# Kernel tuning notes

Hardware: AMD Instinct MI355X
Metric: run time of the kernel (lower is better)

Reference implementation:

```python
import jax, jax.numpy as jnp
import numpy as np

HEAD_NUM = 16
QKV_DIM = 32
EMB = 512
SQRT_EMB = 22.627416997969522  # sqrt(512)
LOGIT_CLIP = 10.0
BATCH, POMO, PROBLEM = 32, 256, 1024


def setup_inputs() -> dict:
    key = jax.random.key(0)
    ks = jax.random.split(key, 8)
    s = 0.02
    return {
        "encoded_nodes": jax.random.normal(ks[0], (BATCH, PROBLEM, EMB), jnp.float32),
        "encoded_q1": jax.random.normal(ks[1], (BATCH, POMO, EMB), jnp.float32),
        "encoded_last_node": jax.random.normal(ks[2], (BATCH, POMO, EMB), jnp.float32),
        "ninf_mask": jnp.zeros((BATCH, POMO, PROBLEM), jnp.float32),
        # weights stored [in, out] so y = x @ W (equiv. to torch Linear with W.T)
        "Wq_first": jax.random.normal(ks[3], (EMB, HEAD_NUM * QKV_DIM), jnp.float32) * s,
        "Wq_last": jax.random.normal(ks[4], (EMB, HEAD_NUM * QKV_DIM), jnp.float32) * s,
        "Wk": jax.random.normal(ks[5], (EMB, HEAD_NUM * QKV_DIM), jnp.float32) * s,
        "Wv": jax.random.normal(ks[6], (EMB, HEAD_NUM * QKV_DIM), jnp.float32) * s,
        "W_combine": jax.random.normal(ks[7], (HEAD_NUM * QKV_DIM, EMB), jnp.float32) * s,
        "b_combine": jnp.zeros((EMB,), jnp.float32),
    }


def _heads(x):
    # [b, n, h*d] -> [b, h, n, d]
    b, n, _ = x.shape
    return x.reshape(b, n, HEAD_NUM, QKV_DIM).transpose(0, 2, 1, 3)


def reference(encoded_nodes, encoded_q1, encoded_last_node, ninf_mask,
              Wq_first, Wq_last, Wk, Wv, W_combine, b_combine):
    # set_kv
    k = _heads(encoded_nodes @ Wk)                     # [b,h,problem,d]
    v = _heads(encoded_nodes @ Wv)                     # [b,h,problem,d]
    single_head_key = encoded_nodes.transpose(0, 2, 1) # [b,emb,problem]
    # set_q1
    q_first = _heads(encoded_q1 @ Wq_first)            # [b,h,pomo,d]
    # forward
    q_last = _heads(encoded_last_node @ Wq_last)       # [b,h,pomo,d]
    q = q_first + q_last

    scale = 1.0 / jnp.sqrt(jnp.asarray(QKV_DIM, q.dtype))
    score = jnp.einsum("bhnd,bhmd->bhnm", q, k) * scale  # [b,h,pomo,problem]
    score = score + ninf_mask[:, None, :, :]
    weights = jax.nn.softmax(score, axis=-1)
    out = jnp.einsum("bhnm,bhmd->bhnd", weights, v)      # [b,h,pomo,d]
    out_concat = out.transpose(0, 2, 1, 3).reshape(q.shape[0], q.shape[2], HEAD_NUM * QKV_DIM)
    mh_out = out_concat @ W_combine + b_combine          # [b,pomo,emb]

    score2 = jnp.einsum("bne,bem->bnm", mh_out, single_head_key) / SQRT_EMB
    score2 = LOGIT_CLIP * jnp.tanh(score2) + ninf_mask
    probs = jax.nn.softmax(score2, axis=2)               # [b,pomo,problem]
    return probs
```

## Files before the change

### kernel.cpp

```cpp
#include <hip/hip_runtime.h>
#include <math.h>

typedef unsigned short u16;
typedef __attribute__((ext_vector_type(8))) short bf16x8;
typedef __attribute__((ext_vector_type(4))) float f32x4;
typedef __attribute__((ext_vector_type(4))) int i32x4;
typedef __attribute__((ext_vector_type(4))) short s16x4;
typedef __attribute__((ext_vector_type(4))) unsigned short u16x4;

#define MFMA16(a,b,c) __builtin_amdgcn_mfma_f32_16x16x32_bf16((a),(b),(c),0,0,0)

__device__ __forceinline__ u16 f2bf(float x){
  unsigned int u = __float_as_uint(x);
  u += 0x7fffu + ((u >> 16) & 1u);
  return (u16)(u >> 16);
}
__device__ __forceinline__ float bf2f(u16 x){
  return __uint_as_float(((unsigned)x) << 16);
}
__device__ __forceinline__ void gload16(const void* g, void* l){
  __builtin_amdgcn_global_load_lds((const __attribute__((address_space(1))) void*)g,
                                   (__attribute__((address_space(3))) void*)l, 16, 0, 0);
}

__global__ __launch_bounds__(256) void prep(
    const float* __restrict__ nodes, const float* __restrict__ q1, const float* __restrict__ lastn,
    const float* __restrict__ mask,
    const float* __restrict__ Wqf, const float* __restrict__ Wql, const float* __restrict__ Wk,
    const float* __restrict__ Wv, const float* __restrict__ Wc,
    u16* __restrict__ qlbP,
    u16* __restrict__ WtKV, u16* __restrict__ WtQ2, u16* __restrict__ WtCP,
    u16* __restrict__ nodesP, u16* __restrict__ maskP)
{
  const int tid = blockIdx.x * 256 + threadIdx.x;

  #pragma unroll
  for (int it = 0; it < 2; ++it) {
    int id = tid + it*1048576;
    int ln = id & 15, q = (id >> 4) & 3, kc = (id >> 6) & 15, cb = (id >> 10) & 63, b = id >> 16;
    const float* s = nodes + ((b*1024 + cb*16 + ln)*512 + kc*32 + q*8);
    float4 v0 = *(const float4*)s, v1 = *(const float4*)(s+4);
    u16 o[8];
    o[0]=f2bf(v0.x); o[1]=f2bf(v0.y); o[2]=f2bf(v0.z); o[3]=f2bf(v0.w);
    o[4]=f2bf(v1.x); o[5]=f2bf(v1.y); o[6]=f2bf(v1.z); o[7]=f2bf(v1.w);
    *(i32x4*)&nodesP[id*8] = *(i32x4*)&o[0];
  }

  {
    int ln = tid & 15, q = (tid >> 4) & 3, kc = (tid >> 6) & 31, mblk = tid >> 11;
    int m = mblk*16 + ln, k = kc*32 + q*8;
    const float* s = (k < 512) ? (q1 + m*512 + k) : (lastn + m*512 + (k - 512));
    float4 v0 = *(const float4*)s, v1 = *(const float4*)(s+4);
    u16 o[8];
    o[0]=f2bf(v0.x); o[1]=f2bf(v0.y); o[2]=f2bf(v0.z); o[3]=f2bf(v0.w);
    o[4]=f2bf(v1.x); o[5]=f2bf(v1.y); o[6]=f2bf(v1.z); o[7]=f2bf(v1.w);
    *(i32x4*)&qlbP[tid*8] = *(i32x4*)&o[0];
  }

  if (tid < 262144) {
    int n = tid >> 9, k = tid & 511;
    WtQ2[n*1024 + k]       = f2bf(Wqf[k*512 + n]);
    WtQ2[n*1024 + 512 + k] = f2bf(Wql[k*512 + n]);
  }
  if (tid < 524288) {
    int n = tid >> 9, k = tid & 511;
    WtKV[tid] = f2bf(n < 512 ? Wk[k*512 + n] : Wv[k*512 + (n-512)]);
  }
  if (tid < 32768) {
    int ln = tid & 15, q = (tid >> 4) & 3, kc = (tid >> 6) & 15, cb = tid >> 10;
    u16 o[8];
    #pragma unroll
    for (int e=0;e<8;e++) o[e] = f2bf(Wc[(kc*32 + q*8 + e)*512 + cb*16 + ln]);
    *(i32x4*)&WtCP[tid*8] = *(i32x4*)&o[0];
  }
  if (tid < 524288) {
    int brt = tid >> 10, c = tid & 1023;
    const float* mp = mask + (brt*16)*1024 + c;
    u16 vals[16];
    #pragma unroll
    for (int p=0;p<16;p++) vals[p] = f2bf(mp[p*1024]);
    u16* dst = maskP + (brt*64 + (c >> 4))*256 + (c & 15)*4;
    #pragma unroll
    for (int q4=0;q4<4;q4++) {
      u16x4 v; v[0]=vals[q4*4]; v[1]=vals[q4*4+1]; v[2]=vals[q4*4+2]; v[3]=vals[q4*4+3];
      *(u16x4*)&dst[q4*64] = v;
    }
  }
}

__global__ __launch_bounds__(512, 2) void kvq(
    const u16* __restrict__ Akv, const u16* __restrict__ Bkv,
    const u16* __restrict__ Aq,  const u16* __restrict__ Bq,
    u16* __restrict__ Kout, u16* __restrict__ Vout, u16* __restrict__ Qout)
{
  __shared__ u16 smem[24576];
  const int t = threadIdx.x, w = t >> 6, l = t & 63, q = l >> 4, ln = l & 15;
  const int wr = w >> 2, wc = w & 3;
  const int wm = wr * 64, wn = wc * 64;

  const bool isq = blockIdx.x < 128;
  int mb, nb, ksteps, kstr, KC;
  const u16 *Ab, *Bb;
  if (isq) {
    const int bid = blockIdx.x;
    mb = bid >> 1; nb = bid & 1;
    ksteps = 32; kstr = 1024; KC = 32; Ab = Aq; Bb = Bq;
  } else {
    const int bid = blockIdx.x - 128;
    mb = (bid >> 5)*8 + (bid & 7);
    nb = (bid >> 3) & 3;
    ksteps = 16; kstr = 512; KC = 16; Ab = Akv; Bb = Bkv;
  }
  const int m0 = mb*128, n0 = nb*256;

  f32x4 acc[4][4];
  #pragma unroll
  for (int i=0;i<4;i++)
    #pragma unroll
    for (int j=0;j<4;j++)
      #pragma unroll
      for (int r=0;r<4;r++) acc[i][j][r] = 0.f;

  const u16* ApL  = Ab + (((m0 >> 4) + (t >> 6))*KC*64 + (t & 63))*8;
  const u16* Baddr = Bb + (n0 + (t & 255))*kstr + (t >> 8)*8;

  #define STAGE(kc_, b_) { \
    u16* s = smem + (b_)*12288; \
    gload16(ApL + (kc_)*512,       &s[t*8]); \
    gload16(Baddr + (kc_)*32,      &s[4096 + t*8]); \
    gload16(Baddr + 16 + (kc_)*32, &s[4096 + (t+512)*8]); }

  STAGE(0, 0);
  for (int kc = 0; kc < ksteps; kc++) {
    __syncthreads();
    if (kc + 1 < ksteps) STAGE(kc+1, (kc+1)&1);
    const u16* sa = smem + (kc&1)*12288;
    const u16* sb = sa + 4096;
    const int acb = wm >> 4;
    bf16x8 af[4], bfr[4];
    #pragma unroll
    for (int i=0;i<4;i++) af[i]  = *(bf16x8*)&sa[((acb + i)*4 + q)*128 + ln*8];
    #pragma unroll
    for (int j=0;j<4;j++) bfr[j] = *(bf16x8*)&sb[(q*256 + wn + j*16 + ln)*8];
    #pragma unroll
    for (int i=0;i<4;i++)
      #pragma unroll
      for (int j=0;j<4;j++)
        acc[i][j] = MFMA16(af[i], bfr[j], acc[i][j]);
  }
  #undef STAGE

  const float scale = isq ? 0.17677669529663687f : 1.0f;
  const int bb_ = mb >> 3, mloc = (mb & 7)*128;
  const int bbq = mb >> 1, pm0 = (mb & 1)*128;
  for (int h = 0; h < 4; ++h) {
    __syncthreads();
    if (wc == h) {
      #pragma unroll
      for (int i=0;i<4;i++)
        #pragma unroll
        for (int j=0;j<4;j++) {
          s16x4 o;
          #pragma unroll
          for (int r=0;r<4;r++) o[r] = (short)f2bf(acc[i][j][r]*scale);
          *(s16x4*)&smem[(j*16 + ln)*140 + wm + i*16 + q*4] = o;
        }
    }
    __syncthreads();
    #pragma unroll
    for (int hc=0; hc<2; ++hc) {
      if (isq) {
        const int head = nb*8 + h*2 + hc;
        const int m_ = t >> 2, d0 = (t & 3)*8;
        u16 v[8];
        #pragma unroll
        for (int dd=0;dd<8;dd++) v[dd] = smem[(hc*32 + d0 + dd)*140 + m_];
        *(i32x4*)&Qout[((bbq*16 + head)*256 + pm0 + m_)*32 + d0] = *(i32x4*)&v[0];
      } else if (nb < 2) {
        const int head = nb*8 + h*2 + hc;
        const int m_ = t >> 2, d0 = (t & 3)*8;
        u16 v[8];
        #pragma unroll
        for (int dd=0;dd<8;dd++) v[dd] = smem[(hc*32 + d0 + dd)*140 + m_];
        *(i32x4*)&Kout[((bb_*16 + head)*1024 + mloc + m_)*32 + d0] = *(i32x4*)&v[0];
      } else {
        const int vh = (nb-2)*8 + h*2 + hc;
        const int d = t >> 4, mo = (t & 15)*8;
        *(i32x4*)&Vout[((bb_*16 + vh)*32 + d)*1024 + mloc + mo]
            = *(i32x4*)&smem[(hc*32 + d)*140 + mo];
      }
    }
  }
}

__global__ __launch_bounds__(256) void attn(const u16* __restrict__ Qg, const u16* __restrict__ Kg,
                                            const u16* __restrict__ Vtg, const u16* __restrict__ maskP,
                                            u16* __restrict__ Og)
{
  const int bid = blockIdx.x;
  const int bh = (bid & 7)*64 + (bid >> 3);
  const int h = bh & 15, bb = bh >> 4;
  const int t = threadIdx.x, w = t >> 6, l = t & 63, q = l >> 4, ln = l & 15;
  __shared__ u16 Qs[8192];
  __shared__ u16 Ks[2][4096];
  __shared__ u16 Vs[2][4096];
  __shared__ u16 Ps[5120];
  u16* PwA = &Ps[w*640];
  u16* PwB = &Ps[2560 + w*640];
  const int qbase = (bb*16 + h)*256*32;
  #pragma unroll
  for (int c=0;c<4;c++)
    gload16(&Qg[qbase + t*32 + c*8], &Qs[(c*256 + t)*8]);
  const int kbase = (bb*16 + h)*1024*32;
  const int vbase = (bb*16 + h)*32*1024;

  #define STAGE_KV(mc_, b_) { \
    gload16(&Kg[kbase + ((mc_)*128 + (t & 127))*32 + (t >> 7)*8],     &Ks[b_][t*8]); \
    gload16(&Kg[kbase + ((mc_)*128 + (t & 127))*32 + ((t >> 7)+2)*8], &Ks[b_][(t+256)*8]); \
    gload16(&Vtg[vbase + (t & 31)*1024 + (mc_)*128 + (t >> 5)*8],     &Vs[b_][t*8]); \
    gload16(&Vtg[vbase + (t & 31)*1024 + (mc_)*128 + ((t >> 5)+8)*8], &Vs[b_][(t+256)*8]); }

  STAGE_KV(0, 0)

  float rs[4][4];
  f32x4 oacc[4][2];
  #pragma unroll
  for (int rg=0;rg<4;rg++) {
    #pragma unroll
    for (int r=0;r<4;r++) rs[rg][r] = 0.f;
    #pragma unroll
    for (int dt=0;dt<2;dt++)
      #pragma unroll
      for (int r=0;r<4;r++) oacc[rg][dt][r] = 0.f;
  }
  __syncthreads();
  bf16x8 aq[4];
  #pragma unroll
  for (int rg=0;rg<4;rg++) aq[rg] = *(bf16x8*)&Qs[(q*256 + w*64 + rg*16 + ln)*8];
  const u16* mbase = maskP + (bb*16 + w*4)*16384 + q*64 + ln*4;
  u16x4 mqA[8], mqB[8];
  #pragma unroll
  for (int j2=0;j2<8;j2++) mqA[j2] = *(const u16x4*)&mbase[j2*256];

  #define RG_BODY(rg, MQC, MQN, PRRG, PRMC) { \
    _Pragma("unroll") \
    for (int j2=0;j2<8;j2++) \
      MQN[j2] = *(const u16x4*)&mbase[(PRRG)*16384 + ((PRMC)*8 + j2)*256]; \
    _Pragma("unroll") \
    for (int ch=0; ch<4; ch++) { \
      u16* Pc = (ch & 1) ? PwB : PwA; \
      bf16x8 bk0 = *(bf16x8*)&Kc[(q*128 + (ch*2+0)*16 + ln)*8]; \
      bf16x8 bk1 = *(bf16x8*)&Kc[(q*128 + (ch*2+1)*16 + ln)*8]; \
      f32x4 zz = {0.f,0.f,0.f,0.f}; \
      f32x4 s0 = MFMA16(aq[rg], bk0, zz); \
      f32x4 s1 = MFMA16(aq[rg], bk1, zz); \
      _Pragma("unroll") \
      for (int r=0;r<4;r++) { \
        float e0 = __expf(s0[r] + bf2f(MQC[ch*2+0][r])); \
        float e1 = __expf(s1[r] + bf2f(MQC[ch*2+1][r])); \
        rs[rg][r] += e0 + e1; \
        Pc[(q*4+r)*40 + ln]      = f2bf(e0); \
        Pc[(q*4+r)*40 + 16 + ln] = f2bf(e1); \
      } \
      bf16x8 ap  = *(bf16x8*)&Pc[ln*40 + q*8]; \
      bf16x8 bv0 = *(bf16x8*)&Vc[((ch*4+q)*32 + ln)*8]; \
      bf16x8 bv1 = *(bf16x8*)&Vc[((ch*4+q)*32 + 16 + ln)*8]; \
      oacc[rg][0] = MFMA16(ap, bv0, oacc[rg][0]); \
      oacc[rg][1] = MFMA16(ap, bv1, oacc[rg][1]); \
    } }

  for (int mc = 0; mc < 8; mc++) {
    if (mc) __syncthreads();
    if (mc < 7) STAGE_KV(mc+1, (mc+1)&1)
    const u16* Kc = Ks[mc&1];
    const u16* Vc = Vs[mc&1];
    RG_BODY(0, mqA, mqB, 1, mc)
    RG_BODY(1, mqB, mqA, 2, mc)
    RG_BODY(2, mqA, mqB, 3, mc)
    RG_BODY(3, mqB, mqA, 0, (mc+1))
  }
  #undef RG_BODY
  #undef STAGE_KV

  #pragma unroll
  for (int rg=0;rg<4;rg++) {
    #pragma unroll
    for (int r=0;r<4;r++) {
      float v = rs[rg][r];
      v += __shfl_xor(v,1); v += __shfl_xor(v,2); v += __shfl_xor(v,4); v += __shfl_xor(v,8);
      rs[rg][r] = __builtin_amdgcn_rcpf(v);
    }
    const int orow = bb*256 + w*64 + rg*16 + q*4;
    #pragma unroll
    for (int dt=0;dt<2;dt++)
      #pragma unroll
      for (int r=0;r<4;r++)
        Og[(orow + r)*512 + h*32 + dt*16 + ln] = f2bf(oacc[rg][dt][r]*rs[rg][r]);
  }
}

__global__ __launch_bounds__(1024) void cmbfin(const u16* __restrict__ oc, const u16* __restrict__ WtCP,
                                               const float* __restrict__ bias,
                                               const u16* __restrict__ nodesP, const u16* __restrict__ maskP,
                                               float* __restrict__ out)
{
  const int bid = blockIdx.x;
  const int bb = bid & 31, rg = bid >> 5;
  const int t = threadIdx.x, w = t >> 6, l = t & 63, q = l >> 4, ln = l & 15;
  __shared__ u16 As[16384];
  __shared__ u16 Ms[16384];
  __shared__ float rsL[16][32];
  const int abase = (bb*256 + rg*32)*512;
  #pragma unroll
  for (int c=0;c<2;c++) {
    int chunk = t + 1024*c;
    gload16(&oc[abase + (chunk & 31)*512 + (chunk >> 5)*8], &As[chunk*8]);
  }
  __syncthreads();
  f32x4 acc1[2][2];
  #pragma unroll
  for (int i=0;i<2;i++)
    #pragma unroll
    for (int ct=0;ct<2;ct++)
      #pragma unroll
      for (int r=0;r<4;r++) acc1[i][ct][r] = 0.f;
  #pragma unroll 4
  for (int kc=0;kc<16;kc++) {
    bf16x8 af[2];
    #pragma unroll
    for (int i=0;i<2;i++) af[i] = *(bf16x8*)&As[((kc*4 + q)*32 + i*16 + ln)*8];
    #pragma unroll
    for (int ct=0;ct<2;ct++) {
      bf16x8 bfr = *(const bf16x8*)&WtCP[(((w*2 + ct)*16 + kc)*4 + q)*128 + ln*8];
      #pragma unroll
      for (int i=0;i<2;i++) acc1[i][ct] = MFMA16(af[i], bfr, acc1[i][ct]);
    }
  }
  #pragma unroll
  for (int ct=0;ct<2;ct++) {
    int gn = w*32 + ct*16 + ln;
    float bv = bias[gn];
    #pragma unroll
    for (int i=0;i<2;i++)
      #pragma unroll
      for (int r=0;r<4;r++)
        Ms[(gn >> 3)*256 + (i*16 + q*4 + r)*8 + (gn & 7)] = f2bf(acc1[i][ct][r] + bv);
  }
  __syncthreads();
  float rloc[2][4] = {{0.f,0.f,0.f,0.f},{0.f,0.f,0.f,0.f}};
  const int nbase = bb*524288;
  f32x4 acc[2][4];
  #pragma unroll
  for (int i=0;i<2;i++)
    #pragma unroll
    for (int ct=0;ct<4;ct++)
      #pragma unroll
      for (int r=0;r<4;r++) acc[i][ct][r] = 0.f;
  #pragma unroll 2
  for (int kc=0;kc<16;kc++) {
    bf16x8 af[2];
    #pragma unroll
    for (int i=0;i<2;i++) af[i] = *(bf16x8*)&Ms[((kc*4 + q)*32 + i*16 + ln)*8];
    #pragma unroll
    for (int ct=0;ct<4;ct++) {
      bf16x8 bfr = *(const bf16x8*)&nodesP[nbase + (((w*4 + ct)*16 + kc)*4 + q)*128 + ln*8];
      #pragma unroll
      for (int i=0;i<2;i++) acc[i][ct] = MFMA16(af[i], bfr, acc[i][ct]);
    }
  }
  const float c2 = 0.08838834764831843f;
  const int prow_base = bb*256 + rg*32;
  #pragma unroll
  for (int i=0;i<2;i++) {
    #pragma unroll
    for (int ct=0;ct<4;ct++) {
      u16x4 mv = *(const u16x4*)&maskP[((bb*16 + rg*2 + i)*64 + w*4 + ct)*256 + q*64 + ln*4];
      #pragma unroll
      for (int r=0;r<4;r++) {
        float x = acc[i][ct][r] * c2;
        x = fminf(fmaxf(x, -30.f), 30.f);
        float e2 = __expf(x);
        float lg = 10.f*(e2 - 1.f)*__builtin_amdgcn_rcpf(e2 + 1.f) + bf2f(mv[r]);
        float e = __expf(lg);
        rloc[i][r] += e;
        acc[i][ct][r] = e;
      }
    }
  }
  #pragma unroll
  for (int i=0;i<2;i++)
    #pragma unroll
    for (int r=0;r<4;r++) {
      float v = rloc[i][r];
      v += __shfl_xor(v,1); v += __shfl_xor(v,2); v += __shfl_xor(v,4); v += __shfl_xor(v,8);
      rloc[i][r] = v;
    }
  if (ln == 0) {
    #pragma unroll
    for (int i=0;i<2;i++)
      #pragma unroll
      for (int r=0;r<4;r++) rsL[w][i*16 + q*4 + r] = rloc[i][r];
  }
  __syncthreads();
  float inv[2][4];
  #pragma unroll
  for (int i=0;i<2;i++)
    #pragma unroll
    for (int r=0;r<4;r++) {
      float tot = 0.f;
      #pragma unroll
      for (int ww=0;ww<16;ww++) tot += rsL[ww][i*16 + q*4 + r];
      inv[i][r] = __builtin_amdgcn_rcpf(tot);
    }
  #pragma unroll
  for (int i=0;i<2;i++)
    #pragma unroll
    for (int ct=0;ct<4;ct++) {
      int col0 = w*64 + ct*16 + ln;
      #pragma unroll
      for (int r=0;r<4;r++)
        out[(prow_base + i*16 + q*4 + r)*1024 + col0] = acc[i][ct][r]*inv[i][r];
    }
}

extern "C" void kernel_launch(void* const* d_in, const int* in_sizes, int n_in,
                              void* d_out, int out_size, void* d_ws, size_t ws_size,
                              hipStream_t stream)
{
  (void)in_sizes; (void)n_in; (void)out_size; (void)ws_size;
  const float* nodes = (const float*)d_in[0];
  const float* q1    = (const float*)d_in[1];
  const float* lastn = (const float*)d_in[2];
  const float* mask  = (const float*)d_in[3];
  const float* Wqf   = (const float*)d_in[4];
  const float* Wql   = (const float*)d_in[5];
  const float* Wk    = (const float*)d_in[6];
  const float* Wv    = (const float*)d_in[7];
  const float* Wc    = (const float*)d_in[8];
  const float* bias  = (const float*)d_in[9];
  float* out = (float*)d_out;

  char* p = (char*)d_ws;
  u16* qlbP   = (u16*)p; p += 16777216;
  u16* WtKV   = (u16*)p; p += 1048576;
  u16* WtQ2   = (u16*)p; p += 1048576;
  u16* WtCP   = (u16*)p; p += 524288;
  u16* nodesP = (u16*)p; p += 33554432;
  u16* maskP  = (u16*)p; p += 16777216;
  u16* Kt     = (u16*)p; p += 33554432;
  u16* Vt     = (u16*)p; p += 33554432;
  u16* Qh     = (u16*)p; p += 8388608;
  u16* oc  = qlbP;

  prep<<<4096, 256, 0, stream>>>(nodes, q1, lastn, mask, Wqf, Wql, Wk, Wv, Wc,
                                 qlbP, WtKV, WtQ2, WtCP, nodesP, maskP);
  kvq<<<1152, 512, 0, stream>>>(nodesP, WtKV, qlbP, WtQ2, Kt, Vt, Qh);
  attn<<<512, 256, 0, stream>>>(Qh, Kt, Vt, maskP, oc);
  cmbfin<<<256, 1024, 0, stream>>>(oc, WtCP, bias, nodesP, maskP, out);
}
```

Before: 338.5 us.

## Triple-buffer kvq GEMM LDS staging with split-phase MFMA and vmcnt waits

The projection GEMM kernel moves from double to triple LDS buffering with a prefetch distance of two k-steps. It replaces __syncthreads with explicit vmcnt/lgkmcnt waits and raw barriers, and splits each k-step into two MFMA halves so the global-to-LDS loads for later steps are issued between them. Wave priority is raised around the MFMA bursts. The goal is to hide global load latency behind matrix math, at the cost of 50% more LDS, which may reduce occupancy, and more fragile hand-written synchronization.

```diff
diff --git a/kernel.cpp b/kernel.cpp
--- a/kernel.cpp
+++ b/kernel.cpp
@@ -93,7 +93,7 @@
     const u16* __restrict__ Aq,  const u16* __restrict__ Bq,
     u16* __restrict__ Kout, u16* __restrict__ Vout, u16* __restrict__ Qout)
 {
-  __shared__ u16 smem[24576];
+  __shared__ u16 smem[36864];
   const int t = threadIdx.x, w = t >> 6, l = t & 63, q = l >> 4, ln = l & 15;
   const int wr = w >> 2, wc = w & 3;
   const int wm = wr * 64, wn = wc * 64;
@@ -121,34 +121,65 @@
       #pragma unroll
       for (int r=0;r<4;r++) acc[i][j][r] = 0.f;
 
-  const u16* ApL  = Ab + (((m0 >> 4) + (t >> 6))*KC*64 + (t & 63))*8;
+  const u16* ApL   = Ab + (((m0 >> 4) + (t >> 6))*KC*64 + (t & 63))*8;
   const u16* Baddr = Bb + (n0 + (t & 255))*kstr + (t >> 8)*8;
 
-  #define STAGE(kc_, b_) { \
-    u16* s = smem + (b_)*12288; \
-    gload16(ApL + (kc_)*512,       &s[t*8]); \
-    gload16(Baddr + (kc_)*32,      &s[4096 + t*8]); \
-    gload16(Baddr + 16 + (kc_)*32, &s[4096 + (t+512)*8]); }
-
-  STAGE(0, 0);
+  #define SG_A(kc_, b_)  gload16(ApL + (kc_)*512,       &smem[(b_)*12288 + t*8]);
+  #define SG_B0(kc_, b_) gload16(Baddr + (kc_)*32,      &smem[(b_)*12288 + 4096 + t*8]);
+  #define SG_B1(kc_, b_) gload16(Baddr + 16 + (kc_)*32, &smem[(b_)*12288 + 4096 + (t+512)*8]);
+
+  SG_A(0, 0) SG_B0(0, 0) SG_B1(0, 0)
+  SG_A(1, 1) SG_B0(1, 1) SG_B1(1, 1)
+
+  int ib = 0;
+  int tb = 2;
+  const int acb = wm >> 4;
   for (int kc = 0; kc < ksteps; kc++) {
-    __syncthreads();
-    if (kc + 1 < ksteps) STAGE(kc+1, (kc+1)&1);
-    const u16* sa = smem + (kc&1)*12288;
+    if (kc + 1 < ksteps) asm volatile("s_waitcnt vmcnt(3)" ::: "memory");
+    else                 asm volatile("s_waitcnt vmcnt(0)" ::: "memory");
+    __builtin_amdgcn_s_barrier();
+
+    const u16* sa = smem + ib*12288;
     const u16* sb = sa + 4096;
-    const int acb = wm >> 4;
-    bf16x8 af[4], bfr[4];
-    #pragma unroll
-    for (int i=0;i<4;i++) af[i]  = *(bf16x8*)&sa[((acb + i)*4 + q)*128 + ln*8];
-    #pragma unroll
-    for (int j=0;j<4;j++) bfr[j] = *(bf16x8*)&sb[(q*256 + wn + j*16 + ln)*8];
-    #pragma unroll
-    for (int i=0;i<4;i++)
-      #pragma unroll
-      for (int j=0;j<4;j++)
-        acc[i][j] = MFMA16(af[i], bfr[j], acc[i][j]);
-  }
-  #undef STAGE
+    const bool more = (kc + 2 < ksteps);
+
+    bf16x8 af[4], b0, b1;
+    #pragma unroll
+    for (int i=0;i<4;i++) af[i] = *(bf16x8*)&sa[((acb + i)*4 + q)*128 + ln*8];
+    b0 = *(bf16x8*)&sb[(q*256 + wn + 0*16 + ln)*8];
+    b1 = *(bf16x8*)&sb[(q*256 + wn + 1*16 + ln)*8];
+    if (more) { SG_A(kc+2, tb) SG_B0(kc+2, tb) }
+    asm volatile("s_waitcnt lgkmcnt(0)" ::: "memory");
+    __builtin_amdgcn_sched_barrier(0);
+    __builtin_amdgcn_s_setprio(1);
+    #pragma unroll
+    for (int i=0;i<4;i++) {
+      acc[i][0] = MFMA16(af[i], b0, acc[i][0]);
+      acc[i][1] = MFMA16(af[i], b1, acc[i][1]);
+    }
+    __builtin_amdgcn_s_setprio(0);
+    __builtin_amdgcn_s_barrier();
+
+    bf16x8 b2, b3;
+    b2 = *(bf16x8*)&sb[(q*256 + wn + 2*16 + ln)*8];
+    b3 = *(bf16x8*)&sb[(q*256 + wn + 3*16 + ln)*8];
+    if (more) { SG_B1(kc+2, tb) }
+    asm volatile("s_waitcnt lgkmcnt(0)" ::: "memory");
+    __builtin_amdgcn_sched_barrier(0);
+    __builtin_amdgcn_s_setprio(1);
+    #pragma unroll
+    for (int i=0;i<4;i++) {
+      acc[i][2] = MFMA16(af[i], b2, acc[i][2]);
+      acc[i][3] = MFMA16(af[i], b3, acc[i][3]);
+    }
+    __builtin_amdgcn_s_setprio(0);
+
+    ib = (ib == 2) ? 0 : ib + 1;
+    tb = (tb == 2) ? 0 : tb + 1;
+  }
+  #undef SG_A
+  #undef SG_B0
+  #undef SG_B1
 
   const float scale = isq ? 0.17677669529663687f : 1.0f;
   const int bb_ = mb >> 3, mloc = (mb & 7)*128;
```

Result: slower. 348.4 us (+2.9%).
